# Performance work log

Hardware: AMD Instinct MI355X
Metric: run time of the kernel (lower is better)

The kernel has to match this reference:

```python
import jax, jax.numpy as jnp
import numpy as np

B, S, D = 4, 2048, 1024
H = 4096          # d_model * hidden_mult
E = 8             # n_experts
TOP_K = 2
AUX_COEF = 0.01


def setup_inputs() -> dict:
    key = jax.random.key(0)
    ks = jax.random.split(key, 5)
    x = jax.random.normal(ks[0], (B, S, D), dtype=jnp.float32)
    router_w = jax.random.normal(ks[1], (D, E), dtype=jnp.float32) * 0.02
    temp = jnp.ones((1,), dtype=jnp.float32)
    Wg = jax.random.normal(ks[2], (E, D, H), dtype=jnp.float32) * 0.02
    Wu = jax.random.normal(ks[3], (E, D, H), dtype=jnp.float32) * 0.02
    Wd = jax.random.normal(ks[4], (E, H, D), dtype=jnp.float32) * 0.02
    return {"x": x, "router_w": router_w, "temp": temp, "Wg": Wg, "Wu": Wu, "Wd": Wd}


def reference(x, router_w, temp, Wg, Wu, Wd):
    # --- Top2Router (eval mode: no jitter noise, no dropout) ---
    t = jnp.clip(temp, 0.1, 5.0)                         # scalar temp param, clamped
    logits = jnp.einsum('bsd,de->bse', x, router_w) / t   # [B,S,E]
    probs = jax.nn.softmax(logits, axis=-1)
    w, idx = jax.lax.top_k(probs, TOP_K)                  # [B,S,K] weights / expert ids

    # --- Expert dispatch / compute / combine ---
    # dropless=True -> no capacity dropping. Tokens not routed to expert e get
    # combine weight 0, so a masked-weight dense accumulate matches the
    # gather->MLP->scatter math of the original exactly.
    out = jnp.zeros_like(x)
    for e in range(E):  # fixed small expert count; structurally distinct weights
        we = jnp.sum(w * (idx == e), axis=-1)             # [B,S] combine weight for expert e
        gate = jnp.einsum('bsd,dh->bsh', x, Wg[e])
        up = jnp.einsum('bsd,dh->bsh', x, Wu[e])
        hidden = jax.nn.silu(up) * gate                   # swiglu: silu(up_proj) * gate_proj
        ye = jnp.einsum('bsh,hd->bsd', hidden, Wd[e])
        out = out + we[..., None] * ye

    # --- Aux losses ---
    importance = probs.mean(axis=(0, 1))                  # [E]
    assigned = jnp.sum(jax.nn.one_hot(idx, E, dtype=probs.dtype), axis=(0, 1, 2))  # [E]
    load = assigned / (B * S + 1e-6)
    aux_load_loss = (importance * load).sum() * E * AUX_COEF
    router_entropy = -(probs * jnp.log(jnp.clip(probs, 1e-8))).sum(-1).mean() * 0.01
    overflow_pct = jnp.zeros((), dtype=x.dtype)           # dropless -> never overflows
    return out, aux_load_loss, router_entropy, overflow_pct
```

## Files before the change

### kernel.cpp

```cpp
#include <hip/hip_runtime.h>
#include <stdint.h>

#define T_TOK 8192
#define D_DIM 1024
#define H_DIM 4096
#define NGU   8192
#define NEXP  8
#define MAX_YT 136

typedef float  f32x4  __attribute__((ext_vector_type(4)));
typedef __bf16 bf16x8 __attribute__((ext_vector_type(8)));
typedef __bf16 bf16x4 __attribute__((ext_vector_type(4)));

__device__ __forceinline__ void gl_lds16(const void* g, void* l) {
  __builtin_amdgcn_global_load_lds(
      (__attribute__((address_space(1))) void*)g,
      (__attribute__((address_space(3))) void*)l, 16u, 0, 0u);
}

__global__ __launch_bounds__(256) void router_kernel(
    const float* __restrict__ x, const float* __restrict__ rw,
    const float* __restrict__ temp,
    int* __restrict__ rowtok, float* __restrict__ rowwt,
    int* __restrict__ cnt, float* __restrict__ imp_part,
    float* __restrict__ ent_part)
{
  const int wid  = threadIdx.x >> 6;
  const int lane = threadIdx.x & 63;
  const int t    = blockIdx.x * 4 + wid;

  float acc[8];
#pragma unroll
  for (int e = 0; e < 8; e++) acc[e] = 0.f;
  const float* xr = x + (size_t)t * D_DIM;
#pragma unroll
  for (int it = 0; it < 16; it++) {
    int d = it * 64 + lane;
    float xv = xr[d];
    const float4 r0 = *(const float4*)(rw + d * 8);
    const float4 r1 = *(const float4*)(rw + d * 8 + 4);
    acc[0] += xv * r0.x; acc[1] += xv * r0.y;
    acc[2] += xv * r0.z; acc[3] += xv * r0.w;
    acc[4] += xv * r1.x; acc[5] += xv * r1.y;
    acc[6] += xv * r1.z; acc[7] += xv * r1.w;
  }
#pragma unroll
  for (int e = 0; e < 8; e++) {
    float v = acc[e];
#pragma unroll
    for (int off = 32; off > 0; off >>= 1) v += __shfl_xor(v, off, 64);
    acc[e] = v;
  }
  float tclamp = fminf(fmaxf(temp[0], 0.1f), 5.0f);
  float invt = 1.0f / tclamp;
  float mx = -1e30f;
#pragma unroll
  for (int e = 0; e < 8; e++) { acc[e] *= invt; mx = fmaxf(mx, acc[e]); }
  float p[8]; float s = 0.f;
#pragma unroll
  for (int e = 0; e < 8; e++) { p[e] = __expf(acc[e] - mx); s += p[e]; }
  float invs = 1.0f / s;
  float ent = 0.f;
#pragma unroll
  for (int e = 0; e < 8; e++) {
    p[e] *= invs;
    ent -= p[e] * __logf(fmaxf(p[e], 1e-8f));
  }
  int i1 = 0; float w1 = p[0];
#pragma unroll
  for (int e = 1; e < 8; e++) if (p[e] > w1) { w1 = p[e]; i1 = e; }
  int i2 = (i1 == 0) ? 1 : 0; float w2 = p[i2];
#pragma unroll
  for (int e = 0; e < 8; e++) if (e != i1 && p[e] > w2) { w2 = p[e]; i2 = e; }

  __shared__ float s_imp[4][8];
  __shared__ float s_ent[4];
  if (lane == 0) {
    int pos1 = atomicAdd(&cnt[i1], 1);
    rowtok[i1 * T_TOK + pos1] = t * 2;
    rowwt [i1 * T_TOK + pos1] = w1;
    int pos2 = atomicAdd(&cnt[i2], 1);
    rowtok[i2 * T_TOK + pos2] = t * 2 + 1;
    rowwt [i2 * T_TOK + pos2] = w2;
#pragma unroll
    for (int e = 0; e < 8; e++) s_imp[wid][e] = p[e];
    s_ent[wid] = ent;
  }
  __syncthreads();
  if (threadIdx.x < 8) {
    int e = threadIdx.x;
    imp_part[blockIdx.x * 8 + e] =
        s_imp[0][e] + s_imp[1][e] + s_imp[2][e] + s_imp[3][e];
  } else if (threadIdx.x == 8) {
    ent_part[blockIdx.x] = s_ent[0] + s_ent[1] + s_ent[2] + s_ent[3];
  }
}

__global__ __launch_bounds__(256) void aux_final_kernel(
    const float* __restrict__ imp_part, const float* __restrict__ ent_part,
    const int* __restrict__ cnt, int* __restrict__ tileoff,
    float* __restrict__ out_aux)
{
  __shared__ float simp[256];
  __shared__ float sent[256];
  int tid = threadIdx.x;
  int e = tid & 7, g = tid >> 3;
  float ia = 0.f;
  for (int b = g; b < 2048; b += 32) ia += imp_part[b * 8 + e];
  simp[tid] = ia;
  float ea = 0.f;
  for (int b = tid; b < 2048; b += 256) ea += ent_part[b];
  sent[tid] = ea;
  __syncthreads();
  if (tid == 0) {
    float imp[8] = {0,0,0,0,0,0,0,0};
    float ent = 0.f;
    for (int i = 0; i < 256; i++) { imp[i & 7] += simp[i]; ent += sent[i]; }
    float aux = 0.f;
    for (int ee = 0; ee < 8; ee++) {
      float importance = imp[ee] / 8192.0f;
      float load = (float)cnt[ee] / (8192.0f + 1e-6f);
      aux += importance * load;
    }
    out_aux[0] = aux * 8.0f * 0.01f;
    out_aux[1] = (ent / 8192.0f) * 0.01f;
    out_aux[2] = 0.f;
    int off = 0;
    for (int ee = 0; ee < 8; ee++) { tileoff[ee] = off; off += (cnt[ee] + 127) >> 7; }
    tileoff[8] = off;
  }
}

__global__ __launch_bounds__(256) void convert_x_kernel(
    const float* __restrict__ x, __bf16* __restrict__ xb)
{
  size_t i = ((size_t)blockIdx.x * 256 + threadIdx.x) * 4;
  float4 v = *(const float4*)(x + i);
  bf16x4 o;
  o[0] = (__bf16)v.x; o[1] = (__bf16)v.y; o[2] = (__bf16)v.z; o[3] = (__bf16)v.w;
  *(bf16x4*)(xb + i) = o;
}

__global__ __launch_bounds__(256) void transpose_gu_kernel(
    const float* __restrict__ Wg, const float* __restrict__ Wu,
    __bf16* __restrict__ BguT)
{
  int e  = blockIdx.z >> 1;
  int up = blockIdx.z & 1;
  const float* src = (up ? Wu : Wg) + (size_t)e * D_DIM * H_DIM;
  int h0 = blockIdx.x * 64, d0 = blockIdx.y * 64;
  __shared__ float tile[64][65];
  int c = threadIdx.x & 63, r4 = threadIdx.x >> 6;
#pragma unroll
  for (int i = 0; i < 16; i++) {
    int r = r4 * 16 + i;
    tile[r][c] = src[(size_t)(d0 + r) * H_DIM + h0 + c];
  }
  __syncthreads();
  __bf16* dst = BguT + (size_t)e * NGU * D_DIM;
#pragma unroll
  for (int i = 0; i < 16; i++) {
    int rr = r4 * 16 + i;
    int h = h0 + rr;
    int nrow = ((h >> 4) << 5) + (h & 15) + (up << 4);
    dst[(size_t)nrow * D_DIM + d0 + c] = (__bf16)tile[c][rr];
  }
}

__global__ __launch_bounds__(256) void transpose_wd_kernel(
    const float* __restrict__ Wd, __bf16* __restrict__ BdT)
{
  int e = blockIdx.z;
  const float* src = Wd + (size_t)e * H_DIM * D_DIM;
  int d0 = blockIdx.x * 64, h0 = blockIdx.y * 64;
  __shared__ float tile[64][65];
  int c = threadIdx.x & 63, r4 = threadIdx.x >> 6;
#pragma unroll
  for (int i = 0; i < 16; i++) {
    int r = r4 * 16 + i;
    tile[r][c] = src[(size_t)(h0 + r) * D_DIM + d0 + c];
  }
  __syncthreads();
  __bf16* dst = BdT + (size_t)e * D_DIM * H_DIM;
#pragma unroll
  for (int i = 0; i < 16; i++) {
    int rr = r4 * 16 + i;
    dst[(size_t)(d0 + rr) * H_DIM + h0 + c] = (__bf16)tile[c][rr];
  }
}

__global__ __launch_bounds__(256, 2) void gemm1_kernel(
    const __bf16* __restrict__ xb, const __bf16* __restrict__ BguT,
    const int* __restrict__ rowtok, const float* __restrict__ rowwt,
    const int* __restrict__ cnt, const int* __restrict__ tileoff,
    __bf16* __restrict__ hid)
{
  __shared__ __bf16 As[128 * 64];
  __shared__ __bf16 Bs[128 * 64];
  __shared__ int   s_tok[128];
  __shared__ float s_wt[128];

  int y = blockIdx.y;
  if (y >= tileoff[8]) return;
  int e = 0;
  while (y >= tileoff[e + 1]) e++;
  int m0 = (y - tileoff[e]) << 7;
  int cntE = cnt[e];
  int tid = threadIdx.x;
  if (tid < 128) {
    int m = m0 + tid;
    bool v = m < cntE;
    s_tok[tid] = v ? rowtok[e * T_TOK + m] : 0;
    s_wt [tid] = v ? rowwt [e * T_TOK + m] : 0.f;
  }
  __syncthreads();

  const int n0 = blockIdx.x << 7;
  const __bf16* Bp = BguT + (size_t)e * NGU * D_DIM;
  const int lane = tid & 63;
  const int wid = tid >> 6;
  const int wm = wid >> 1, wn = wid & 1;
  const int l15 = lane & 15, l4 = lane >> 4;

  f32x4 zero = {0.f, 0.f, 0.f, 0.f};
  f32x4 acc[4][4];
#pragma unroll
  for (int a = 0; a < 4; a++)
#pragma unroll
    for (int b = 0; b < 4; b++) acc[a][b] = zero;

  int q[4], ar[4], akc[4];
#pragma unroll
  for (int c = 0; c < 4; c++) {
    q[c]   = tid + (c << 8);
    ar[c]  = q[c] >> 3;
    akc[c] = ((q[c] & 7) ^ (ar[c] & 7)) << 3;
  }

  for (int kt = 0; kt < 16; kt++) {
    int k0 = kt << 6;
#pragma unroll
    for (int c = 0; c < 4; c++) {
      const __bf16* ga = xb + (size_t)(s_tok[ar[c]] >> 1) * D_DIM + (k0 + akc[c]);
      gl_lds16(ga, &As[q[c] << 3]);
    }
#pragma unroll
    for (int c = 0; c < 4; c++) {
      const __bf16* gb = Bp + (size_t)(n0 + ar[c]) * D_DIM + (k0 + akc[c]);
      gl_lds16(gb, &Bs[q[c] << 3]);
    }
    __syncthreads();
#pragma unroll
    for (int ks = 0; ks < 2; ks++) {
      bf16x8 af[4], bfv[4];
#pragma unroll
      for (int mi = 0; mi < 4; mi++) {
        int row = wm * 64 + mi * 16 + l15;
        int kidx = (ks * 4 + l4) ^ (row & 7);
        af[mi] = *(const bf16x8*)&As[(row * 8 + kidx) * 8];
      }
#pragma unroll
      for (int ni = 0; ni < 4; ni++) {
        int row = wn * 64 + ni * 16 + l15;
        int kidx = (ks * 4 + l4) ^ (row & 7);
        bfv[ni] = *(const bf16x8*)&Bs[(row * 8 + kidx) * 8];
      }
#pragma unroll
      for (int mi = 0; mi < 4; mi++)
#pragma unroll
        for (int ni = 0; ni < 4; ni++)
          acc[mi][ni] = __builtin_amdgcn_mfma_f32_16x16x32_bf16(
              af[mi], bfv[ni], acc[mi][ni], 0, 0, 0);
    }
    __syncthreads();
  }

#pragma unroll
  for (int mi = 0; mi < 4; mi++) {
#pragma unroll
    for (int p2 = 0; p2 < 2; p2++) {
      f32x4 gt = acc[mi][2 * p2];
      f32x4 up = acc[mi][2 * p2 + 1];
      int nb = n0 + wn * 64 + p2 * 32;
      int h = ((nb >> 5) << 4) + l15;
#pragma unroll
      for (int r = 0; r < 4; r++) {
        int rl = wm * 64 + mi * 16 + l4 * 4 + r;
        if (m0 + rl < cntE) {
          float u = up[r];
          float hv = (u / (1.f + __expf(-u))) * gt[r] * s_wt[rl];
          hid[(size_t)s_tok[rl] * H_DIM + h] = (__bf16)hv;
        }
      }
    }
  }
}

__global__ __launch_bounds__(256, 2) void gemm2_kernel(
    const __bf16* __restrict__ hid, const __bf16* __restrict__ BdT,
    const int* __restrict__ rowtok, const int* __restrict__ cnt,
    const int* __restrict__ tileoff, float* __restrict__ out)
{
  __shared__ __bf16 As[128 * 64];
  __shared__ __bf16 Bs[128 * 64];
  __shared__ int s_tok[128];

  int y = blockIdx.y;
  if (y >= tileoff[8]) return;
  int e = 0;
  while (y >= tileoff[e + 1]) e++;
  int m0 = (y - tileoff[e]) << 7;
  int cntE = cnt[e];
  int tid = threadIdx.x;
  if (tid < 128) {
    int m = m0 + tid;
    s_tok[tid] = (m < cntE) ? rowtok[e * T_TOK + m] : 0;
  }
  __syncthreads();

  const int n0 = blockIdx.x << 7;
  const __bf16* Bp = BdT + (size_t)e * D_DIM * H_DIM;
  const int lane = tid & 63;
  const int wid = tid >> 6;
  const int wm = wid >> 1, wn = wid & 1;
  const int l15 = lane & 15, l4 = lane >> 4;

  f32x4 zero = {0.f, 0.f, 0.f, 0.f};
  f32x4 acc[4][4];
#pragma unroll
  for (int a = 0; a < 4; a++)
#pragma unroll
    for (int b = 0; b < 4; b++) acc[a][b] = zero;

  int q[4], ar[4], akc[4];
#pragma unroll
  for (int c = 0; c < 4; c++) {
    q[c]   = tid + (c << 8);
    ar[c]  = q[c] >> 3;
    akc[c] = ((q[c] & 7) ^ (ar[c] & 7)) << 3;
  }

  for (int kt = 0; kt < 64; kt++) {
    int k0 = kt << 6;
#pragma unroll
    for (int c = 0; c < 4; c++) {
      const __bf16* ga = hid + (size_t)s_tok[ar[c]] * H_DIM + (k0 + akc[c]);
      gl_lds16(ga, &As[q[c] << 3]);
    }
#pragma unroll
    for (int c = 0; c < 4; c++) {
      const __bf16* gb = Bp + (size_t)(n0 + ar[c]) * H_DIM + (k0 + akc[c]);
      gl_lds16(gb, &Bs[q[c] << 3]);
    }
    __syncthreads();
#pragma unroll
    for (int ks = 0; ks < 2; ks++) {
      bf16x8 af[4], bfv[4];
#pragma unroll
      for (int mi = 0; mi < 4; mi++) {
        int row = wm * 64 + mi * 16 + l15;
        int kidx = (ks * 4 + l4) ^ (row & 7);
        af[mi] = *(const bf16x8*)&As[(row * 8 + kidx) * 8];
      }
#pragma unroll
      for (int ni = 0; ni < 4; ni++) {
        int row = wn * 64 + ni * 16 + l15;
        int kidx = (ks * 4 + l4) ^ (row & 7);
        bfv[ni] = *(const bf16x8*)&Bs[(row * 8 + kidx) * 8];
      }
#pragma unroll
      for (int mi = 0; mi < 4; mi++)
#pragma unroll
        for (int ni = 0; ni < 4; ni++)
          acc[mi][ni] = __builtin_amdgcn_mfma_f32_16x16x32_bf16(
              af[mi], bfv[ni], acc[mi][ni], 0, 0, 0);
    }
    __syncthreads();
  }

#pragma unroll
  for (int mi = 0; mi < 4; mi++)
#pragma unroll
    for (int ni = 0; ni < 4; ni++) {
      int coln = n0 + wn * 64 + ni * 16 + l15;
#pragma unroll
      for (int r = 0; r < 4; r++) {
        int rl = wm * 64 + mi * 16 + l4 * 4 + r;
        if (m0 + rl < cntE)
          atomicAdd(&out[(size_t)(s_tok[rl] >> 1) * D_DIM + coln], acc[mi][ni][r]);
      }
    }
}

extern "C" void kernel_launch(void* const* d_in, const int* in_sizes, int n_in,
                              void* d_out, int out_size, void* d_ws, size_t ws_size,
                              hipStream_t stream)
{
  const float* x    = (const float*)d_in[0];
  const float* rw   = (const float*)d_in[1];
  const float* temp = (const float*)d_in[2];
  const float* Wg   = (const float*)d_in[3];
  const float* Wu   = (const float*)d_in[4];
  const float* Wd   = (const float*)d_in[5];
  float* out = (float*)d_out;

  char* ws = (char*)d_ws;
  size_t off = 0;
  auto alloc = [&](size_t bytes) -> void* {
    void* p = ws + off;
    off = (off + bytes + 255) & ~(size_t)255;
    return p;
  };
  __bf16* xb     = (__bf16*)alloc((size_t)T_TOK * D_DIM * 2);
  __bf16* BguT   = (__bf16*)alloc((size_t)NEXP * NGU * D_DIM * 2);
  __bf16* BdT    = (__bf16*)alloc((size_t)NEXP * D_DIM * H_DIM * 2);
  __bf16* hid    = (__bf16*)alloc((size_t)T_TOK * 2 * H_DIM * 2);
  int*    rowtok = (int*)  alloc((size_t)NEXP * T_TOK * 4);
  float*  rowwt  = (float*)alloc((size_t)NEXP * T_TOK * 4);
  int*    cnt    = (int*)  alloc(64);
  int*    tileoff= (int*)  alloc(64);
  float*  imp_part = (float*)alloc(2048 * 8 * 4);
  float*  ent_part = (float*)alloc(2048 * 4);
  (void)ws_size; (void)n_in; (void)in_sizes;

  hipMemsetAsync(d_out, 0, (size_t)out_size * 4, stream);
  hipMemsetAsync(cnt, 0, 64, stream);

  router_kernel<<<2048, 256, 0, stream>>>(x, rw, temp, rowtok, rowwt, cnt,
                                          imp_part, ent_part);
  aux_final_kernel<<<1, 256, 0, stream>>>(imp_part, ent_part, cnt, tileoff,
                                          out + (size_t)T_TOK * D_DIM);
  convert_x_kernel<<<8192, 256, 0, stream>>>(x, xb);
  transpose_gu_kernel<<<dim3(64, 16, 16), 256, 0, stream>>>(Wg, Wu, BguT);
  transpose_wd_kernel<<<dim3(16, 64, 8), 256, 0, stream>>>(Wd, BdT);
  gemm1_kernel<<<dim3(64, MAX_YT), 256, 0, stream>>>(xb, BguT, rowtok, rowwt,
                                                     cnt, tileoff, hid);
  gemm2_kernel<<<dim3(8, MAX_YT), 256, 0, stream>>>(hid, BdT, rowtok, cnt,
                                                    tileoff, out);
}
```

Baseline: 1.156 ms.

## Fuse x conversion into router, merge weight transposes, replace atomics with combine pass

The fp32-to-bf16 conversion of x moves into the router kernel, which now reads x with float4 loads, so x is read from memory once instead of twice. The two weight transpose kernels are merged into a single kernel that uses vectorized float4 loads and writes 8 bf16 values per store. gemm2 now writes per-(token,slot) rows into a scratch buffer that aliases the BguT workspace, and a new combine kernel sums the two slots per token. This removes the float atomics and the output memset, at the cost of an extra 64MB write and read. The aliasing is only safe because gemm1 has finished using BguT before gemm2 runs.

```diff
diff --git a/kernel.cpp b/kernel.cpp
--- a/kernel.cpp
+++ b/kernel.cpp
@@ -20,7 +20,7 @@
 
 __global__ __launch_bounds__(256) void router_kernel(
     const float* __restrict__ x, const float* __restrict__ rw,
-    const float* __restrict__ temp,
+    const float* __restrict__ temp, __bf16* __restrict__ xb,
     int* __restrict__ rowtok, float* __restrict__ rowwt,
     int* __restrict__ cnt, float* __restrict__ imp_part,
     float* __restrict__ ent_part)
@@ -34,15 +34,24 @@
   for (int e = 0; e < 8; e++) acc[e] = 0.f;
   const float* xr = x + (size_t)t * D_DIM;
 #pragma unroll
-  for (int it = 0; it < 16; it++) {
-    int d = it * 64 + lane;
-    float xv = xr[d];
-    const float4 r0 = *(const float4*)(rw + d * 8);
-    const float4 r1 = *(const float4*)(rw + d * 8 + 4);
-    acc[0] += xv * r0.x; acc[1] += xv * r0.y;
-    acc[2] += xv * r0.z; acc[3] += xv * r0.w;
-    acc[4] += xv * r1.x; acc[5] += xv * r1.y;
-    acc[6] += xv * r1.z; acc[7] += xv * r1.w;
+  for (int it = 0; it < 4; it++) {
+    int d = (it * 64 + lane) * 4;
+    float4 v = *(const float4*)(xr + d);
+    bf16x4 o;
+    o[0] = (__bf16)v.x; o[1] = (__bf16)v.y;
+    o[2] = (__bf16)v.z; o[3] = (__bf16)v.w;
+    *(bf16x4*)(xb + (size_t)t * D_DIM + d) = o;
+    float vv[4] = {v.x, v.y, v.z, v.w};
+#pragma unroll
+    for (int j = 0; j < 4; j++) {
+      float xv = vv[j];
+      const float4 r0 = *(const float4*)(rw + (d + j) * 8);
+      const float4 r1 = *(const float4*)(rw + (d + j) * 8 + 4);
+      acc[0] += xv * r0.x; acc[1] += xv * r0.y;
+      acc[2] += xv * r0.z; acc[3] += xv * r0.w;
+      acc[4] += xv * r1.x; acc[5] += xv * r1.y;
+      acc[6] += xv * r1.z; acc[7] += xv * r1.w;
+    }
   }
 #pragma unroll
   for (int e = 0; e < 8; e++) {
@@ -131,61 +140,51 @@
   }
 }
 
-__global__ __launch_bounds__(256) void convert_x_kernel(
-    const float* __restrict__ x, __bf16* __restrict__ xb)
-{
-  size_t i = ((size_t)blockIdx.x * 256 + threadIdx.x) * 4;
-  float4 v = *(const float4*)(x + i);
-  bf16x4 o;
-  o[0] = (__bf16)v.x; o[1] = (__bf16)v.y; o[2] = (__bf16)v.z; o[3] = (__bf16)v.w;
-  *(bf16x4*)(xb + i) = o;
-}
-
-__global__ __launch_bounds__(256) void transpose_gu_kernel(
+__global__ __launch_bounds__(256) void transpose_all_kernel(
     const float* __restrict__ Wg, const float* __restrict__ Wu,
-    __bf16* __restrict__ BguT)
-{
-  int e  = blockIdx.z >> 1;
-  int up = blockIdx.z & 1;
-  const float* src = (up ? Wu : Wg) + (size_t)e * D_DIM * H_DIM;
-  int h0 = blockIdx.x * 64, d0 = blockIdx.y * 64;
-  __shared__ float tile[64][65];
-  int c = threadIdx.x & 63, r4 = threadIdx.x >> 6;
-#pragma unroll
-  for (int i = 0; i < 16; i++) {
-    int r = r4 * 16 + i;
-    tile[r][c] = src[(size_t)(d0 + r) * H_DIM + h0 + c];
+    const float* __restrict__ Wd,
+    __bf16* __restrict__ BguT, __bf16* __restrict__ BdT)
+{
+  __shared__ float tile[64 * 129];
+  int z = blockIdx.z;
+  const float* src; __bf16* dst;
+  int C, Kd, r0, c0, up = 0;
+  bool gu = z < 16;
+  if (gu) {
+    int e = z >> 1; up = z & 1;
+    src = (up ? Wu : Wg) + (size_t)e * D_DIM * H_DIM;
+    dst = BguT + (size_t)e * NGU * D_DIM;
+    C = H_DIM; Kd = D_DIM;
+    c0 = (blockIdx.x & 31) << 7;  r0 = (blockIdx.x >> 5) << 6;
+  } else {
+    int e = z - 16;
+    src = Wd + (size_t)e * H_DIM * D_DIM;
+    dst = BdT + (size_t)e * D_DIM * H_DIM;
+    C = D_DIM; Kd = H_DIM;
+    c0 = (blockIdx.x & 7) << 7;   r0 = (blockIdx.x >> 3) << 6;
+  }
+  int t = threadIdx.x;
+  int cq = t & 31, rb = t >> 5;
+#pragma unroll
+  for (int i = 0; i < 8; i++) {
+    int r = rb + 8 * i;
+    float4 v = *(const float4*)(src + (size_t)(r0 + r) * C + c0 + cq * 4);
+    *(float4*)&tile[r * 129 + cq * 4] = v;
   }
   __syncthreads();
-  __bf16* dst = BguT + (size_t)e * NGU * D_DIM;
-#pragma unroll
-  for (int i = 0; i < 16; i++) {
-    int rr = r4 * 16 + i;
-    int h = h0 + rr;
-    int nrow = ((h >> 4) << 5) + (h & 15) + (up << 4);
-    dst[(size_t)nrow * D_DIM + d0 + c] = (__bf16)tile[c][rr];
-  }
-}
-
-__global__ __launch_bounds__(256) void transpose_wd_kernel(
-    const float* __restrict__ Wd, __bf16* __restrict__ BdT)
-{
-  int e = blockIdx.z;
-  const float* src = Wd + (size_t)e * H_DIM * D_DIM;
-  int d0 = blockIdx.x * 64, h0 = blockIdx.y * 64;
-  __shared__ float tile[64][65];
-  int c = threadIdx.x & 63, r4 = threadIdx.x >> 6;
-#pragma unroll
-  for (int i = 0; i < 16; i++) {
-    int r = r4 * 16 + i;
-    tile[r][c] = src[(size_t)(h0 + r) * D_DIM + d0 + c];
-  }
-  __syncthreads();
-  __bf16* dst = BdT + (size_t)e * D_DIM * H_DIM;
-#pragma unroll
-  for (int i = 0; i < 16; i++) {
-    int rr = r4 * 16 + i;
-    dst[(size_t)(d0 + rr) * H_DIM + h0 + c] = (__bf16)tile[c][rr];
+#pragma unroll
+  for (int i = 0; i < 4; i++) {
+    int c = t + (i << 8);
+    int hl = c >> 3;
+    int rc = c & 7;
+    int dstrow;
+    if (gu) { int h = c0 + hl; dstrow = ((h >> 4) << 5) + (h & 15) + (up << 4); }
+    else    { dstrow = c0 + hl; }
+    bf16x8 o;
+#pragma unroll
+    for (int j = 0; j < 8; j++)
+      o[j] = (__bf16)tile[(rc * 8 + j) * 129 + hl];
+    *(bf16x8*)(dst + (size_t)dstrow * Kd + r0 + rc * 8) = o;
   }
 }
 
@@ -299,7 +298,7 @@
 __global__ __launch_bounds__(256, 2) void gemm2_kernel(
     const __bf16* __restrict__ hid, const __bf16* __restrict__ BdT,
     const int* __restrict__ rowtok, const int* __restrict__ cnt,
-    const int* __restrict__ tileoff, float* __restrict__ out)
+    const int* __restrict__ tileoff, float* __restrict__ ytmp)
 {
   __shared__ __bf16 As[128 * 64];
   __shared__ __bf16 Bs[128 * 64];
@@ -387,9 +386,21 @@
       for (int r = 0; r < 4; r++) {
         int rl = wm * 64 + mi * 16 + l4 * 4 + r;
         if (m0 + rl < cntE)
-          atomicAdd(&out[(size_t)(s_tok[rl] >> 1) * D_DIM + coln], acc[mi][ni][r]);
-      }
-    }
+          ytmp[(size_t)s_tok[rl] * D_DIM + coln] = acc[mi][ni][r];
+      }
+    }
+}
+
+__global__ __launch_bounds__(256) void combine_kernel(
+    const float* __restrict__ ytmp, float* __restrict__ out)
+{
+  size_t i = ((size_t)blockIdx.x * 256 + threadIdx.x) * 4;
+  size_t t = i >> 10;
+  size_t col = i & 1023;
+  const float4 a = *(const float4*)(ytmp + ((t * 2) << 10) + col);
+  const float4 b = *(const float4*)(ytmp + ((t * 2 + 1) << 10) + col);
+  float4 o = {a.x + b.x, a.y + b.y, a.z + b.z, a.w + b.w};
+  *(float4*)(out + i) = o;
 }
 
 extern "C" void kernel_launch(void* const* d_in, const int* in_sizes, int n_in,
@@ -421,20 +432,20 @@
   int*    tileoff= (int*)  alloc(64);
   float*  imp_part = (float*)alloc(2048 * 8 * 4);
   float*  ent_part = (float*)alloc(2048 * 4);
+  float* ytmp = (float*)BguT;
   (void)ws_size; (void)n_in; (void)in_sizes;
 
-  hipMemsetAsync(d_out, 0, (size_t)out_size * 4, stream);
   hipMemsetAsync(cnt, 0, 64, stream);
 
-  router_kernel<<<2048, 256, 0, stream>>>(x, rw, temp, rowtok, rowwt, cnt,
+  router_kernel<<<2048, 256, 0, stream>>>(x, rw, temp, xb, rowtok, rowwt, cnt,
                                           imp_part, ent_part);
   aux_final_kernel<<<1, 256, 0, stream>>>(imp_part, ent_part, cnt, tileoff,
                                           out + (size_t)T_TOK * D_DIM);
-  convert_x_kernel<<<8192, 256, 0, stream>>>(x, xb);
-  transpose_gu_kernel<<<dim3(64, 16, 16), 256, 0, stream>>>(Wg, Wu, BguT);
-  transpose_wd_kernel<<<dim3(16, 64, 8), 256, 0, stream>>>(Wd, BdT);
+  transpose_all_kernel<<<dim3(512, 1, 24), 256, 0, stream>>>(Wg, Wu, Wd,
+                                                             BguT, BdT);
   gemm1_kernel<<<dim3(64, MAX_YT), 256, 0, stream>>>(xb, BguT, rowtok, rowwt,
                                                      cnt, tileoff, hid);
   gemm2_kernel<<<dim3(8, MAX_YT), 256, 0, stream>>>(hid, BdT, rowtok, cnt,
-                                                    tileoff, out);
-}
+                                                    tileoff, ytmp);
+  combine_kernel<<<8192, 256, 0, stream>>>(ytmp, out);
+}
```

Result: faster. 1.123 ms (-2.8%).
